# Kernel optimization log

Measured on AMD Instinct MI355X. Metric: run time of the kernel, lower is better.

The kernel has to match this reference:

```python
import jax, jax.numpy as jnp
import numpy as np

T, D, E, K = 16384, 4096, 64, 8
GUMBEL_TAU = 1.0
ROUTER_TEMP = 1.0
SELECT_TEMP = None  # falls back to router_temp, as in the module
EPS = 1e-06


def setup_inputs() -> dict:
    key = jax.random.key(0)
    k1, k2, k3 = jax.random.split(key, 3)
    h = jax.random.normal(k1, (T, D), dtype=jnp.float32)
    # eqx.nn.Linear weight: shape (out_features, in_features), uniform init scale
    W = jax.random.normal(k2, (E, D), dtype=jnp.float32) * (1.0 / np.sqrt(D))
    # uniform noise for Gumbel, matching minval=1e-6, maxval=1-1e-6
    u = jax.random.uniform(k3, (T, E), minval=EPS, maxval=1.0 - EPS, dtype=jnp.float32)
    return {"h": h, "W": W, "u": u}


def reference(h, W, u):
    # logits_clean = vmap(Linear)(h) = h @ W.T, shape (T, E)
    logits_clean = jnp.einsum("td,ed->te", h, W)

    t_mix = jnp.clip(jnp.float32(ROUTER_TEMP), EPS, None)
    probs = jax.nn.softmax(logits_clean / t_mix, axis=-1)

    sel_temp = ROUTER_TEMP if SELECT_TEMP is None else SELECT_TEMP
    t_sel = jnp.clip(jnp.float32(sel_temp), EPS, None)
    logits_sel = logits_clean / t_sel

    # training path: Gumbel noise g = -log(-log(u))
    g = -jnp.log(-jnp.log(u))
    logits_sel = logits_sel + GUMBEL_TAU * g

    # hard top-k mask per row (scatter of ones at top-k indices == one_hot().sum())
    _, idx = jax.lax.top_k(logits_sel, K)  # (T, K)
    rows = jnp.arange(logits_sel.shape[0])[:, None]
    mask_full = jnp.zeros(logits_sel.shape, dtype=bool).at[rows, idx].set(True)

    return (mask_full, probs, logits_clean, logits_sel)
```

## Files before the change

### kernel.cpp

```cpp
#include <hip/hip_runtime.h>
#include <hip/hip_bf16.h>
#include <math.h>
#include <stdint.h>

#define T_ROWS 16384
#define D_DIM  4096
#define E_EXP  64
#define TOPK   8

constexpr float W_SCALE   = 64.0f;
constexpr float INV_SCALE = 1.0f / 64.0f;

constexpr int BM   = 64;
constexpr int BK   = 32;
constexpr int KQ   = D_DIM / 4;
constexpr int NIT  = KQ / BK;
constexpr int ABUF = 8192;
constexpr int BBUF = 8192;
constexpr int B_OFF = 3 * ABUF;
constexpr int LDS_TOT = B_OFF + 2 * BBUF;

typedef _Float16 f16x8 __attribute__((ext_vector_type(8)));
typedef __fp16   h16x2 __attribute__((ext_vector_type(2)));
typedef float    f32x4 __attribute__((ext_vector_type(4)));

__device__ __forceinline__ void gll16(const void* g, void* l) {
    __builtin_amdgcn_global_load_lds(
        (const __attribute__((address_space(1))) void*)g,
        (__attribute__((address_space(3))) void*)l, 16, 0, 0);
}
#define WAITV(n) asm volatile("s_waitcnt vmcnt(" #n ")" ::: "memory")
#define SB0()    __builtin_amdgcn_sched_barrier(0)

__global__ __launch_bounds__(256) void wprep_kernel(
    const float* __restrict__ W, _Float16* __restrict__ Wt)
{
    const int i  = blockIdx.x * 256 + threadIdx.x;
    const int e  = i >> 9;
    const int k8 = i & 511;
    const int k  = k8 << 3;
    const int t  = k >> 5;
    const int s  = (k >> 3) & 3;
    const float4 w0 = *(const float4*)&W[(size_t)e * D_DIM + k];
    const float4 w1 = *(const float4*)&W[(size_t)e * D_DIM + k + 4];
    const float xs[8] = {w0.x, w0.y, w0.z, w0.w, w1.x, w1.y, w1.z, w1.w};
    f16x8 hi, lo;
    #pragma unroll
    for (int j = 0; j < 8; ++j) {
        const float x = xs[j] * W_SCALE;
        const _Float16 hh = (_Float16)x;
        hi[j] = hh;
        lo[j] = (_Float16)(x - (float)hh);
    }
    const size_t o = (size_t)t * 4096 + e * 32 + ((s ^ (e & 3)) << 3);
    *(f16x8*)(Wt + o) = hi;
    *(f16x8*)(Wt + o + 2048) = lo;
}

__device__ __forceinline__ void cvt8(const float4 x0, const float4 x1,
                                     f16x8& hi, f16x8& lo) {
    const float xs[8] = {x0.x, x0.y, x0.z, x0.w, x1.x, x1.y, x1.z, x1.w};
    float hs[8], ls[8];
    #pragma unroll
    for (int j = 0; j < 8; ++j) {
        hs[j] = __uint_as_float(__float_as_uint(xs[j]) & 0xFFFFE000u);
        ls[j] = xs[j] - hs[j];
    }
    #pragma unroll
    for (int j = 0; j < 4; ++j) {
        const h16x2 ph = __builtin_amdgcn_cvt_pkrtz(hs[2 * j], hs[2 * j + 1]);
        const h16x2 pl = __builtin_amdgcn_cvt_pkrtz(ls[2 * j], ls[2 * j + 1]);
        hi[2 * j] = (_Float16)ph[0]; hi[2 * j + 1] = (_Float16)ph[1];
        lo[2 * j] = (_Float16)pl[0]; lo[2 * j + 1] = (_Float16)pl[1];
    }
}

__global__ __launch_bounds__(256, 4) void gemm_q_kernel(
    const float* __restrict__ h, const _Float16* __restrict__ Wt,
    float* __restrict__ out)
{
    __shared__ char smb[LDS_TOT];

    const int tid  = threadIdx.x;
    const int wv   = tid >> 6;
    const int lane = tid & 63;
    const int l15  = lane & 15;
    const int kg   = lane >> 4;
    const int wm   = wv >> 1;
    const int we   = wv & 1;
    const int row0 = blockIdx.x * BM;
    const int q    = blockIdx.y;
    const int kb   = q * KQ;

    const char* gA[2]; int lA[2];
    #pragma unroll
    for (int p = 0; p < 2; ++p) {
        const int row = wv * 16 + p * 8 + (lane >> 3);
        gA[p] = (const char*)h + ((size_t)(row0 + row) * D_DIM + kb) * 4
                + (((lane & 7) ^ (lane >> 3)) << 4);
        lA[p] = wv * 2048 + p * 1024;
    }
    const char* gB = (const char*)Wt + (size_t)(q * 32) * 8192
                     + wv * 2048 + lane * 16;
    const int lB = wv * 2048;

    int aro[2][2];
    #pragma unroll
    for (int f = 0; f < 2; ++f)
        #pragma unroll
        for (int qq = 0; qq < 2; ++qq)
            aro[f][qq] = (f * 32 + wm * 16 + l15) * 128
                       + (((kg * 2 + qq) ^ (l15 & 7)) << 4);
    int bro[2][2];
    #pragma unroll
    for (int sel = 0; sel < 2; ++sel)
        #pragma unroll
        for (int es = 0; es < 2; ++es) {
            const int e = we * 32 + es * 16 + l15;
            bro[sel][es] = sel * 4096 + e * 64 + ((kg ^ (e & 3)) << 4);
        }

    f32x4 acc[2][2] = {};
    float4 av[2][2];
    f16x8 bhf[2], blf[2];

    int aCur = 0, aNxt = ABUF, aStg = 2 * ABUF;

    #define STAGE_A(t, aAdd)                                          \
        { _Pragma("unroll")                                           \
          for (int p = 0; p < 2; ++p)                                 \
              gll16(gA[p] + (size_t)(t) * 128, smb + (aAdd) + lA[p]); }
    #define STAGE_B(t, par)                                           \
        { gll16(gB + (size_t)(t) * 8192,        smb + B_OFF + (par) * BBUF + lB); \
          gll16(gB + (size_t)(t) * 8192 + 1024, smb + B_OFF + (par) * BBUF + lB + 1024); }

    #define DSREAD(aAdd, par)                                                 \
        { _Pragma("unroll")                                                   \
          for (int f = 0; f < 2; ++f) {                                       \
              av[f][0] = *(const float4*)(smb + (aAdd) + aro[f][0]);          \
              av[f][1] = *(const float4*)(smb + (aAdd) + aro[f][1]);          \
          }                                                                   \
          _Pragma("unroll")                                                   \
          for (int es = 0; es < 2; ++es) {                                    \
              bhf[es] = *(const f16x8*)(smb + B_OFF + (par) * BBUF + bro[0][es]); \
              blf[es] = *(const f16x8*)(smb + B_OFF + (par) * BBUF + bro[1][es]); \
          } }

    #define MFMAS()                                                           \
        { f16x8 ah[2], al[2];                                                 \
          cvt8(av[0][0], av[0][1], ah[0], al[0]);                             \
          cvt8(av[1][0], av[1][1], ah[1], al[1]);                             \
          _Pragma("unroll")                                                   \
          for (int f = 0; f < 2; ++f)                                         \
              _Pragma("unroll")                                               \
              for (int es = 0; es < 2; ++es) {                                \
                  acc[f][es] = __builtin_amdgcn_mfma_f32_16x16x32_f16(ah[f], bhf[es], acc[f][es], 0, 0, 0); \
                  acc[f][es] = __builtin_amdgcn_mfma_f32_16x16x32_f16(ah[f], blf[es], acc[f][es], 0, 0, 0); \
                  acc[f][es] = __builtin_amdgcn_mfma_f32_16x16x32_f16(al[f], bhf[es], acc[f][es], 0, 0, 0); \
              } }

    #define ROT() { int t_ = aCur; aCur = aNxt; aNxt = aStg; aStg = t_; }

    STAGE_A(0, aCur)
    SB0();
    STAGE_B(0, 0)
    SB0();
    STAGE_A(1, aNxt)
    SB0();
    WAITV(2);
    SB0();
    __builtin_amdgcn_s_barrier();

    for (int i = 0; i < NIT - 2; ++i) {
        DSREAD(aCur, i & 1)
        STAGE_B(i + 1, (i + 1) & 1)
        SB0();
        STAGE_A(i + 2, aStg)
        SB0();
        __builtin_amdgcn_s_setprio(1);
        MFMAS()
        __builtin_amdgcn_s_setprio(0);
        WAITV(2);
        SB0();
        __builtin_amdgcn_s_barrier();
        ROT();
    }
    DSREAD(aCur, (NIT - 2) & 1)
    STAGE_B(NIT - 1, (NIT - 1) & 1)
    SB0();
    MFMAS()
    WAITV(0);
    SB0();
    __builtin_amdgcn_s_barrier();
    ROT();
    DSREAD(aCur, (NIT - 1) & 1)
    MFMAS()

    float* slot = out + (size_t)q * T_ROWS * E_EXP;
    #pragma unroll
    for (int f = 0; f < 2; ++f)
        #pragma unroll
        for (int es = 0; es < 2; ++es)
            #pragma unroll
            for (int r = 0; r < 4; ++r)
                slot[(size_t)(row0 + f * 32 + wm * 16 + kg * 4 + r) * E_EXP
                     + we * 32 + es * 16 + l15] = acc[f][es][r];
}

__global__ __launch_bounds__(256) void epilogue_kernel(
    const float* __restrict__ u, float* __restrict__ out)
{
    const int row  = blockIdx.x * 4 + (threadIdx.x >> 6);
    const int lane = threadIdx.x & 63;
    const size_t te = (size_t)T_ROWS * E_EXP;
    const size_t idx = (size_t)row * E_EXP + lane;

    const float p0 = out[0 * te + idx];
    const float p1 = out[1 * te + idx];
    const float p2 = out[2 * te + idx];
    const float p3 = out[3 * te + idx];
    const float val = (((p0 + p1) + p2) + p3) * INV_SCALE;

    out[2 * te + idx] = val;

    float m = val;
    #pragma unroll
    for (int off = 32; off; off >>= 1) m = fmaxf(m, __shfl_xor(m, off));
    const float p = expf(val - m);
    float ssum = p;
    #pragma unroll
    for (int off = 32; off; off >>= 1) ssum += __shfl_xor(ssum, off);
    out[1 * te + idx] = p / ssum;

    const float uv = u[idx];
    const float g = -logf(-logf(uv));
    const float sel = val + g;
    out[3 * te + idx] = sel;

    float v = sel;
    bool chosen = false;
    #pragma unroll
    for (int itk = 0; itk < TOPK; ++itk) {
        float mv = v;
        #pragma unroll
        for (int off = 32; off; off >>= 1) mv = fmaxf(mv, __shfl_xor(mv, off));
        const unsigned long long b = __ballot(v == mv);
        const int sl = __ffsll((long long)b) - 1;
        if (lane == sl) { chosen = true; v = -INFINITY; }
    }
    out[idx] = chosen ? 1.0f : 0.0f;
}

extern "C" void kernel_launch(void* const* d_in, const int* in_sizes, int n_in,
                              void* d_out, int out_size, void* d_ws, size_t ws_size,
                              hipStream_t stream) {
    const float* h = (const float*)d_in[0];
    const float* W = (const float*)d_in[1];
    const float* u = (const float*)d_in[2];
    float* out = (float*)d_out;

    _Float16* Wt = (_Float16*)d_ws;

    hipLaunchKernelGGL(wprep_kernel, dim3(E_EXP * D_DIM / 8 / 256), dim3(256),
                       0, stream, W, Wt);
    hipLaunchKernelGGL(gemm_q_kernel, dim3(T_ROWS / BM, 4), dim3(256),
                       0, stream, h, Wt, out);
    hipLaunchKernelGGL(epilogue_kernel, dim3(T_ROWS / 4), dim3(256),
                       0, stream, u, out);
}
```

Measured before the change: 78.72 us.

## Double-buffer MFMA operands in registers, prefetching the next LDS tile during MFMAs

```diff
diff --git a/kernel.cpp b/kernel.cpp
--- a/kernel.cpp
+++ b/kernel.cpp
@@ -95,8 +95,8 @@
     const char* gA[2]; int lA[2];
     #pragma unroll
     for (int p = 0; p < 2; ++p) {
-        const int row = wv * 16 + p * 8 + (lane >> 3);
-        gA[p] = (const char*)h + ((size_t)(row0 + row) * D_DIM + kb) * 4
+        gA[p] = (const char*)h
+                + ((size_t)(row0 + wv * 16 + p * 8 + (lane >> 3)) * D_DIM + kb) * 4
                 + (((lane & 7) ^ (lane >> 3)) << 4);
         lA[p] = wv * 2048 + p * 1024;
     }
@@ -121,8 +121,8 @@
         }
 
     f32x4 acc[2][2] = {};
-    float4 av[2][2];
-    f16x8 bhf[2], blf[2];
+    f16x8 Xah0, Xal0, Xah1, Xal1, Xbh0, Xbh1, Xbl0, Xbl1;
+    f16x8 Yah0, Yal0, Yah1, Yal1, Ybh0, Ybh1, Ybl0, Ybl1;
 
     int aCur = 0, aNxt = ABUF, aStg = 2 * ABUF;
 
@@ -134,30 +134,31 @@
         { gll16(gB + (size_t)(t) * 8192,        smb + B_OFF + (par) * BBUF + lB); \
           gll16(gB + (size_t)(t) * 8192 + 1024, smb + B_OFF + (par) * BBUF + lB + 1024); }
 
-    #define DSREAD(aAdd, par)                                                 \
-        { _Pragma("unroll")                                                   \
-          for (int f = 0; f < 2; ++f) {                                       \
-              av[f][0] = *(const float4*)(smb + (aAdd) + aro[f][0]);          \
-              av[f][1] = *(const float4*)(smb + (aAdd) + aro[f][1]);          \
-          }                                                                   \
-          _Pragma("unroll")                                                   \
-          for (int es = 0; es < 2; ++es) {                                    \
-              bhf[es] = *(const f16x8*)(smb + B_OFF + (par) * BBUF + bro[0][es]); \
-              blf[es] = *(const f16x8*)(smb + B_OFF + (par) * BBUF + bro[1][es]); \
-          } }
-
-    #define MFMAS()                                                           \
-        { f16x8 ah[2], al[2];                                                 \
-          cvt8(av[0][0], av[0][1], ah[0], al[0]);                             \
-          cvt8(av[1][0], av[1][1], ah[1], al[1]);                             \
-          _Pragma("unroll")                                                   \
-          for (int f = 0; f < 2; ++f)                                         \
-              _Pragma("unroll")                                               \
-              for (int es = 0; es < 2; ++es) {                                \
-                  acc[f][es] = __builtin_amdgcn_mfma_f32_16x16x32_f16(ah[f], bhf[es], acc[f][es], 0, 0, 0); \
-                  acc[f][es] = __builtin_amdgcn_mfma_f32_16x16x32_f16(ah[f], blf[es], acc[f][es], 0, 0, 0); \
-                  acc[f][es] = __builtin_amdgcn_mfma_f32_16x16x32_f16(al[f], bhf[es], acc[f][es], 0, 0, 0); \
-              } }
+    #define DSREADCVT(S, aAdd, par)                                            \
+        { const float4 a00 = *(const float4*)(smb + (aAdd) + aro[0][0]);       \
+          const float4 a01 = *(const float4*)(smb + (aAdd) + aro[0][1]);       \
+          const float4 a10 = *(const float4*)(smb + (aAdd) + aro[1][0]);       \
+          const float4 a11 = *(const float4*)(smb + (aAdd) + aro[1][1]);       \
+          S##bh0 = *(const f16x8*)(smb + B_OFF + (par) * BBUF + bro[0][0]);    \
+          S##bh1 = *(const f16x8*)(smb + B_OFF + (par) * BBUF + bro[0][1]);    \
+          S##bl0 = *(const f16x8*)(smb + B_OFF + (par) * BBUF + bro[1][0]);    \
+          S##bl1 = *(const f16x8*)(smb + B_OFF + (par) * BBUF + bro[1][1]);    \
+          cvt8(a00, a01, S##ah0, S##al0);                                      \
+          cvt8(a10, a11, S##ah1, S##al1); }
+
+    #define MFMAS(S)                                                           \
+        acc[0][0] = __builtin_amdgcn_mfma_f32_16x16x32_f16(S##ah0, S##bh0, acc[0][0], 0, 0, 0); \
+        acc[0][0] = __builtin_amdgcn_mfma_f32_16x16x32_f16(S##ah0, S##bl0, acc[0][0], 0, 0, 0); \
+        acc[0][0] = __builtin_amdgcn_mfma_f32_16x16x32_f16(S##al0, S##bh0, acc[0][0], 0, 0, 0); \
+        acc[0][1] = __builtin_amdgcn_mfma_f32_16x16x32_f16(S##ah0, S##bh1, acc[0][1], 0, 0, 0); \
+        acc[0][1] = __builtin_amdgcn_mfma_f32_16x16x32_f16(S##ah0, S##bl1, acc[0][1], 0, 0, 0); \
+        acc[0][1] = __builtin_amdgcn_mfma_f32_16x16x32_f16(S##al0, S##bh1, acc[0][1], 0, 0, 0); \
+        acc[1][0] = __builtin_amdgcn_mfma_f32_16x16x32_f16(S##ah1, S##bh0, acc[1][0], 0, 0, 0); \
+        acc[1][0] = __builtin_amdgcn_mfma_f32_16x16x32_f16(S##ah1, S##bl0, acc[1][0], 0, 0, 0); \
+        acc[1][0] = __builtin_amdgcn_mfma_f32_16x16x32_f16(S##al1, S##bh0, acc[1][0], 0, 0, 0); \
+        acc[1][1] = __builtin_amdgcn_mfma_f32_16x16x32_f16(S##ah1, S##bh1, acc[1][1], 0, 0, 0); \
+        acc[1][1] = __builtin_amdgcn_mfma_f32_16x16x32_f16(S##ah1, S##bl1, acc[1][1], 0, 0, 0); \
+        acc[1][1] = __builtin_amdgcn_mfma_f32_16x16x32_f16(S##al1, S##bh1, acc[1][1], 0, 0, 0);
 
     #define ROT() { int t_ = aCur; aCur = aNxt; aNxt = aStg; aStg = t_; }
 
@@ -170,31 +171,43 @@
     WAITV(2);
     SB0();
     __builtin_amdgcn_s_barrier();
-
-    for (int i = 0; i < NIT - 2; ++i) {
-        DSREAD(aCur, i & 1)
+    DSREADCVT(X, aCur, 0)
+
+    for (int i = 0; i < NIT - 2; i += 2) {
         STAGE_B(i + 1, (i + 1) & 1)
         SB0();
         STAGE_A(i + 2, aStg)
         SB0();
+        WAITV(2);
+        SB0();
+        __builtin_amdgcn_s_barrier();
         __builtin_amdgcn_s_setprio(1);
-        MFMAS()
+        MFMAS(X)
+        DSREADCVT(Y, aNxt, (i + 1) & 1)
         __builtin_amdgcn_s_setprio(0);
+        ROT();
+
+        STAGE_B(i + 2, (i + 2) & 1)
+        SB0();
+        STAGE_A(i + 3, aStg)
+        SB0();
         WAITV(2);
         SB0();
         __builtin_amdgcn_s_barrier();
+        __builtin_amdgcn_s_setprio(1);
+        MFMAS(Y)
+        DSREADCVT(X, aNxt, (i + 2) & 1)
+        __builtin_amdgcn_s_setprio(0);
         ROT();
     }
-    DSREAD(aCur, (NIT - 2) & 1)
     STAGE_B(NIT - 1, (NIT - 1) & 1)
     SB0();
-    MFMAS()
     WAITV(0);
     SB0();
     __builtin_amdgcn_s_barrier();
-    ROT();
-    DSREAD(aCur, (NIT - 1) & 1)
-    MFMAS()
+    MFMAS(X)
+    DSREADCVT(Y, aNxt, (NIT - 1) & 1)
+    MFMAS(Y)
 
     float* slot = out + (size_t)q * T_ROWS * E_EXP;
     #pragma unroll
```

New measurement: 83.10 us. 1.06x slower.

## Load B operand straight from global into registers, bypassing LDS staging

Applied to the files above, without the earlier changes.

```diff
diff --git a/kernel.cpp b/kernel.cpp
--- a/kernel.cpp
+++ b/kernel.cpp
@@ -16,13 +16,12 @@
 constexpr int KQ   = D_DIM / 4;
 constexpr int NIT  = KQ / BK;
 constexpr int ABUF = 8192;
-constexpr int BBUF = 8192;
-constexpr int B_OFF = 3 * ABUF;
-constexpr int LDS_TOT = B_OFF + 2 * BBUF;
-
-typedef _Float16 f16x8 __attribute__((ext_vector_type(8)));
-typedef __fp16   h16x2 __attribute__((ext_vector_type(2)));
-typedef float    f32x4 __attribute__((ext_vector_type(4)));
+constexpr int LDS_TOT = 3 * ABUF;
+
+typedef _Float16     f16x8  __attribute__((ext_vector_type(8)));
+typedef __fp16       h16x2  __attribute__((ext_vector_type(2)));
+typedef float        f32x4  __attribute__((ext_vector_type(4)));
+typedef unsigned int ui32x4 __attribute__((ext_vector_type(4)));
 
 __device__ __forceinline__ void gll16(const void* g, void* l) {
     __builtin_amdgcn_global_load_lds(
@@ -52,7 +51,7 @@
         hi[j] = hh;
         lo[j] = (_Float16)(x - (float)hh);
     }
-    const size_t o = (size_t)t * 4096 + e * 32 + ((s ^ (e & 3)) << 3);
+    const size_t o = (size_t)t * 4096 + e * 32 + s * 8;
     *(f16x8*)(Wt + o) = hi;
     *(f16x8*)(Wt + o + 2048) = lo;
 }
@@ -95,14 +94,11 @@
     const char* gA[2]; int lA[2];
     #pragma unroll
     for (int p = 0; p < 2; ++p) {
-        const int row = wv * 16 + p * 8 + (lane >> 3);
-        gA[p] = (const char*)h + ((size_t)(row0 + row) * D_DIM + kb) * 4
+        gA[p] = (const char*)h
+                + ((size_t)(row0 + wv * 16 + p * 8 + (lane >> 3)) * D_DIM + kb) * 4
                 + (((lane & 7) ^ (lane >> 3)) << 4);
         lA[p] = wv * 2048 + p * 1024;
     }
-    const char* gB = (const char*)Wt + (size_t)(q * 32) * 8192
-                     + wv * 2048 + lane * 16;
-    const int lB = wv * 2048;
 
     int aro[2][2];
     #pragma unroll
@@ -111,18 +107,14 @@
         for (int qq = 0; qq < 2; ++qq)
             aro[f][qq] = (f * 32 + wm * 16 + l15) * 128
                        + (((kg * 2 + qq) ^ (l15 & 7)) << 4);
-    int bro[2][2];
-    #pragma unroll
-    for (int sel = 0; sel < 2; ++sel)
-        #pragma unroll
-        for (int es = 0; es < 2; ++es) {
-            const int e = we * 32 + es * 16 + l15;
-            bro[sel][es] = sel * 4096 + e * 64 + ((kg ^ (e & 3)) << 4);
-        }
+
+    const char* bp = (const char*)Wt + (size_t)(q * 32) * 8192
+                     + (we * 32 + l15) * 64 + kg * 16;
 
     f32x4 acc[2][2] = {};
     float4 av[2][2];
-    f16x8 bhf[2], blf[2];
+    ui32x4 b0h0, b0h1, b0l0, b0l1;
+    ui32x4 b1h0, b1h1, b1l0, b1l1;
 
     int aCur = 0, aNxt = ABUF, aStg = 2 * ABUF;
 
@@ -130,40 +122,47 @@
         { _Pragma("unroll")                                           \
           for (int p = 0; p < 2; ++p)                                 \
               gll16(gA[p] + (size_t)(t) * 128, smb + (aAdd) + lA[p]); }
-    #define STAGE_B(t, par)                                           \
-        { gll16(gB + (size_t)(t) * 8192,        smb + B_OFF + (par) * BBUF + lB); \
-          gll16(gB + (size_t)(t) * 8192 + 1024, smb + B_OFF + (par) * BBUF + lB + 1024); }
-
-    #define DSREAD(aAdd, par)                                                 \
+
+    #define LOADB(t, R)                                                        \
+        { const char* p0_ = bp + (size_t)(t) * 8192;                           \
+          asm volatile("global_load_dwordx4 %0, %1, off" : "=v"(R##h0) : "v"(p0_)); \
+          asm volatile("global_load_dwordx4 %0, %1, off" : "=v"(R##h1) : "v"(p0_ + 1024)); \
+          asm volatile("global_load_dwordx4 %0, %1, off" : "=v"(R##l0) : "v"(p0_ + 4096)); \
+          asm volatile("global_load_dwordx4 %0, %1, off" : "=v"(R##l1) : "v"(p0_ + 5120)); }
+
+    #define DSREAD(aAdd)                                                      \
         { _Pragma("unroll")                                                   \
           for (int f = 0; f < 2; ++f) {                                       \
               av[f][0] = *(const float4*)(smb + (aAdd) + aro[f][0]);          \
               av[f][1] = *(const float4*)(smb + (aAdd) + aro[f][1]);          \
-          }                                                                   \
-          _Pragma("unroll")                                                   \
-          for (int es = 0; es < 2; ++es) {                                    \
-              bhf[es] = *(const f16x8*)(smb + B_OFF + (par) * BBUF + bro[0][es]); \
-              blf[es] = *(const f16x8*)(smb + B_OFF + (par) * BBUF + bro[1][es]); \
           } }
 
-    #define MFMAS()                                                           \
-        { f16x8 ah[2], al[2];                                                 \
-          cvt8(av[0][0], av[0][1], ah[0], al[0]);                             \
-          cvt8(av[1][0], av[1][1], ah[1], al[1]);                             \
-          _Pragma("unroll")                                                   \
-          for (int f = 0; f < 2; ++f)                                         \
-              _Pragma("unroll")                                               \
-              for (int es = 0; es < 2; ++es) {                                \
-                  acc[f][es] = __builtin_amdgcn_mfma_f32_16x16x32_f16(ah[f], bhf[es], acc[f][es], 0, 0, 0); \
-                  acc[f][es] = __builtin_amdgcn_mfma_f32_16x16x32_f16(ah[f], blf[es], acc[f][es], 0, 0, 0); \
-                  acc[f][es] = __builtin_amdgcn_mfma_f32_16x16x32_f16(al[f], bhf[es], acc[f][es], 0, 0, 0); \
-              } }
+    #define MFMAS(R)                                                          \
+        { f16x8 ah0, al0, ah1, al1;                                           \
+          cvt8(av[0][0], av[0][1], ah0, al0);                                 \
+          cvt8(av[1][0], av[1][1], ah1, al1);                                 \
+          const f16x8 bh0_ = __builtin_bit_cast(f16x8, R##h0);                \
+          const f16x8 bh1_ = __builtin_bit_cast(f16x8, R##h1);                \
+          const f16x8 bl0_ = __builtin_bit_cast(f16x8, R##l0);                \
+          const f16x8 bl1_ = __builtin_bit_cast(f16x8, R##l1);                \
+          acc[0][0] = __builtin_amdgcn_mfma_f32_16x16x32_f16(ah0, bh0_, acc[0][0], 0, 0, 0); \
+          acc[0][0] = __builtin_amdgcn_mfma_f32_16x16x32_f16(ah0, bl0_, acc[0][0], 0, 0, 0); \
+          acc[0][0] = __builtin_amdgcn_mfma_f32_16x16x32_f16(al0, bh0_, acc[0][0], 0, 0, 0); \
+          acc[0][1] = __builtin_amdgcn_mfma_f32_16x16x32_f16(ah0, bh1_, acc[0][1], 0, 0, 0); \
+          acc[0][1] = __builtin_amdgcn_mfma_f32_16x16x32_f16(ah0, bl1_, acc[0][1], 0, 0, 0); \
+          acc[0][1] = __builtin_amdgcn_mfma_f32_16x16x32_f16(al0, bh1_, acc[0][1], 0, 0, 0); \
+          acc[1][0] = __builtin_amdgcn_mfma_f32_16x16x32_f16(ah1, bh0_, acc[1][0], 0, 0, 0); \
+          acc[1][0] = __builtin_amdgcn_mfma_f32_16x16x32_f16(ah1, bl0_, acc[1][0], 0, 0, 0); \
+          acc[1][0] = __builtin_amdgcn_mfma_f32_16x16x32_f16(al1, bh0_, acc[1][0], 0, 0, 0); \
+          acc[1][1] = __builtin_amdgcn_mfma_f32_16x16x32_f16(ah1, bh1_, acc[1][1], 0, 0, 0); \
+          acc[1][1] = __builtin_amdgcn_mfma_f32_16x16x32_f16(ah1, bl1_, acc[1][1], 0, 0, 0); \
+          acc[1][1] = __builtin_amdgcn_mfma_f32_16x16x32_f16(al1, bh1_, acc[1][1], 0, 0, 0); }
 
     #define ROT() { int t_ = aCur; aCur = aNxt; aNxt = aStg; aStg = t_; }
 
     STAGE_A(0, aCur)
     SB0();
-    STAGE_B(0, 0)
+    LOADB(0, b0)
     SB0();
     STAGE_A(1, aNxt)
     SB0();
@@ -171,30 +170,45 @@
     SB0();
     __builtin_amdgcn_s_barrier();
 
-    for (int i = 0; i < NIT - 2; ++i) {
-        DSREAD(aCur, i & 1)
-        STAGE_B(i + 1, (i + 1) & 1)
+    for (int i = 0; i < NIT - 2; i += 2) {
+        DSREAD(aCur)
+        LOADB(i + 1, b1)
         SB0();
         STAGE_A(i + 2, aStg)
         SB0();
         __builtin_amdgcn_s_setprio(1);
-        MFMAS()
+        MFMAS(b0)
         __builtin_amdgcn_s_setprio(0);
         WAITV(2);
         SB0();
         __builtin_amdgcn_s_barrier();
         ROT();
-    }
-    DSREAD(aCur, (NIT - 2) & 1)
-    STAGE_B(NIT - 1, (NIT - 1) & 1)
-    SB0();
-    MFMAS()
+
+        DSREAD(aCur)
+        LOADB(i + 2, b0)
+        SB0();
+        STAGE_A(i + 3, aStg)
+        SB0();
+        __builtin_amdgcn_s_setprio(1);
+        MFMAS(b1)
+        __builtin_amdgcn_s_setprio(0);
+        WAITV(2);
+        SB0();
+        __builtin_amdgcn_s_barrier();
+        ROT();
+    }
+    DSREAD(aCur)
+    LOADB(NIT - 1, b1)
+    SB0();
+    __builtin_amdgcn_s_setprio(1);
+    MFMAS(b0)
+    __builtin_amdgcn_s_setprio(0);
     WAITV(0);
     SB0();
     __builtin_amdgcn_s_barrier();
     ROT();
-    DSREAD(aCur, (NIT - 1) & 1)
-    MFMAS()
+    DSREAD(aCur)
+    MFMAS(b1)
 
     float* slot = out + (size_t)q * T_ROWS * E_EXP;
     #pragma unroll
```

Result: slower. 86.60 us (+10.0%).
